# Kernel optimization log

Measured on AMD Instinct MI355X. Metric: run time of the kernel, lower is better.

Reference implementation:

```python
import jax, jax.numpy as jnp
import numpy as np

EPS = 1e-08
N_CODECS = 1024

def setup_inputs() -> dict:
    key = jax.random.key(0)
    indices = jax.random.randint(key, (16, 1048576), 0, N_CODECS, dtype=jnp.int64 if jax.config.jax_enable_x64 else jnp.int32)
    return {"indices": indices}

def reference(indices) -> jnp.ndarray:
    # Faithful to: encodings = eq(arange[:,None], flat[None,:]); probs = mean(encodings, dim=1)
    # mean of one-hot over N == count/N, so use a histogram (bincount) instead of the
    # O(n_codecs x N) boolean matrix.
    flat = indices.reshape(-1)
    counts = jnp.bincount(flat, length=N_CODECS)  # [n_codecs]
    probs = counts.astype(jnp.float32) / flat.shape[0]
    perplexity = jnp.exp(-jnp.sum(probs * jnp.log(probs + EPS)))
    return perplexity
```

## Files before the change

kernel.cpp:

```cpp
#include <hip/hip_runtime.h>
#include <hip/hip_bf16.h>

#define N_CODECS 1024
#define EPS 1e-8f

__global__ void zero_bins_kernel(unsigned int* __restrict__ gcounts) {
    int i = blockIdx.x * blockDim.x + threadIdx.x;
    if (i < N_CODECS) gcounts[i] = 0u;
}

__global__ void __launch_bounds__(256) hist_kernel(
        const int* __restrict__ idx,
        unsigned int* __restrict__ gcounts,
        int n4 ) {
    __shared__ unsigned int lcounts[N_CODECS];
    for (int i = threadIdx.x; i < N_CODECS; i += blockDim.x) lcounts[i] = 0u;
    __syncthreads();

    const int4* __restrict__ idx4 = (const int4*)idx;
    int stride = gridDim.x * blockDim.x;
    for (int i = blockIdx.x * blockDim.x + threadIdx.x; i < n4; i += stride) {
        int4 v = idx4[i];
        atomicAdd(&lcounts[v.x], 1u);
        atomicAdd(&lcounts[v.y], 1u);
        atomicAdd(&lcounts[v.z], 1u);
        atomicAdd(&lcounts[v.w], 1u);
    }
    __syncthreads();

    for (int i = threadIdx.x; i < N_CODECS; i += blockDim.x) {
        unsigned int c = lcounts[i];
        if (c) atomicAdd(&gcounts[i], c);
    }
}

__global__ void __launch_bounds__(1024) finalize_kernel(
        const unsigned int* __restrict__ gcounts,
        float* __restrict__ out,
        float invN) {
    int t = threadIdx.x;
    float p = (float)gcounts[t] * invN;
    float term = p * logf(p + EPS);

    #pragma unroll
    for (int off = 32; off > 0; off >>= 1) {
        term += __shfl_down(term, off, 64);
    }

    __shared__ float wsum[16];
    int wave = t >> 6;
    int lane = t & 63;
    if (lane == 0) wsum[wave] = term;
    __syncthreads();

    if (wave == 0) {
        float s = (lane < 16) ? wsum[lane] : 0.0f;
        #pragma unroll
        for (int off = 8; off > 0; off >>= 1) {
            s += __shfl_down(s, off, 64);
        }
        if (lane == 0) out[0] = expf(-s);
    }
}

extern "C" void kernel_launch(void* const* d_in, const int* in_sizes, int n_in,
                              void* d_out, int out_size, void* d_ws, size_t ws_size,
                              hipStream_t stream) {
    const int* indices = (const int*)d_in[0];
    int n = in_sizes[0];
    float* out = (float*)d_out;
    unsigned int* gcounts = (unsigned int*)d_ws;

    int n4 = n >> 2;

    zero_bins_kernel<<<(N_CODECS + 255) / 256, 256, 0, stream>>>(gcounts);

    hist_kernel<<<1024, 256, 0, stream>>>(indices, gcounts, n4);

    finalize_kernel<<<1, 1024, 0, stream>>>(gcounts, out, 1.0f / (float)n);
}
```

Measured before the change: 106.6 us.

## Replace global atomic merge with per-block partial histograms and tree reduction

Each histogram block now writes its full shared-memory histogram to its own slot in the workspace, with no global atomics. A new reduce kernel sums 64 partials per chunk into 16 chunk histograms, and finalize adds those 16. This drops the zero-bins launch and the contention from 1024 blocks atomically updating the same 1024 global counters. In exchange it writes 4 MB of partials, adds a reduction kernel launch, and needs a larger workspace.

```diff
diff --git a/kernel.cpp b/kernel.cpp
--- a/kernel.cpp
+++ b/kernel.cpp
@@ -3,23 +3,20 @@
 
 #define N_CODECS 1024
 #define EPS 1e-8f
+#define HIST_BLOCKS 1024
+#define CHUNKS 16
 
-__global__ void zero_bins_kernel(unsigned int* __restrict__ gcounts) {
-    int i = blockIdx.x * blockDim.x + threadIdx.x;
-    if (i < N_CODECS) gcounts[i] = 0u;
-}
-
-__global__ void __launch_bounds__(256) hist_kernel(
+__global__ void __launch_bounds__(256) hist_partial_kernel(
         const int* __restrict__ idx,
-        unsigned int* __restrict__ gcounts,
-        int n4 ) {
+        unsigned int* __restrict__ gpart,
+        int n4) {
     __shared__ unsigned int lcounts[N_CODECS];
-    for (int i = threadIdx.x; i < N_CODECS; i += blockDim.x) lcounts[i] = 0u;
+    for (int i = threadIdx.x; i < N_CODECS; i += 256) lcounts[i] = 0u;
     __syncthreads();
 
     const int4* __restrict__ idx4 = (const int4*)idx;
-    int stride = gridDim.x * blockDim.x;
-    for (int i = blockIdx.x * blockDim.x + threadIdx.x; i < n4; i += stride) {
+    int stride = gridDim.x * 256;
+    for (int i = blockIdx.x * 256 + threadIdx.x; i < n4; i += stride) {
         int4 v = idx4[i];
         atomicAdd(&lcounts[v.x], 1u);
         atomicAdd(&lcounts[v.y], 1u);
@@ -28,24 +25,47 @@
     }
     __syncthreads();
 
-    for (int i = threadIdx.x; i < N_CODECS; i += blockDim.x) {
-        unsigned int c = lcounts[i];
-        if (c) atomicAdd(&gcounts[i], c);
+    unsigned int* __restrict__ mypart = gpart + (size_t)blockIdx.x * N_CODECS;
+    #pragma unroll
+    for (int i = 0; i < N_CODECS / 256; ++i) {
+        int b = i * 256 + threadIdx.x;
+        mypart[b] = lcounts[b];
     }
 }
 
+__global__ void __launch_bounds__(256) reduce_kernel(
+        const unsigned int* __restrict__ gpart,
+        unsigned int* __restrict__ p2) {
+    int c = blockIdx.x >> 2;
+    int q = blockIdx.x & 3;
+    int bin = q * 256 + threadIdx.x;
+
+    const unsigned int* __restrict__ base = gpart + (size_t)(c * 64) * N_CODECS + bin;
+    unsigned int s0 = 0, s1 = 0, s2 = 0, s3 = 0;
+    #pragma unroll 4
+    for (int k = 0; k < 64; k += 4) {
+        s0 += base[(size_t)(k + 0) * N_CODECS];
+        s1 += base[(size_t)(k + 1) * N_CODECS];
+        s2 += base[(size_t)(k + 2) * N_CODECS];
+        s3 += base[(size_t)(k + 3) * N_CODECS];
+    }
+    p2[c * N_CODECS + bin] = s0 + s1 + s2 + s3;
+}
+
 __global__ void __launch_bounds__(1024) finalize_kernel(
-        const unsigned int* __restrict__ gcounts,
+        const unsigned int* __restrict__ p2,
         float* __restrict__ out,
         float invN) {
     int t = threadIdx.x;
-    float p = (float)gcounts[t] * invN;
+    unsigned int cnt = 0;
+    #pragma unroll
+    for (int c = 0; c < CHUNKS; ++c) cnt += p2[c * N_CODECS + t];
+
+    float p = (float)cnt * invN;
     float term = p * logf(p + EPS);
 
     #pragma unroll
-    for (int off = 32; off > 0; off >>= 1) {
-        term += __shfl_down(term, off, 64);
-    }
+    for (int off = 32; off > 0; off >>= 1) term += __shfl_down(term, off, 64);
 
     __shared__ float wsum[16];
     int wave = t >> 6;
@@ -56,9 +76,7 @@
     if (wave == 0) {
         float s = (lane < 16) ? wsum[lane] : 0.0f;
         #pragma unroll
-        for (int off = 8; off > 0; off >>= 1) {
-            s += __shfl_down(s, off, 64);
-        }
+        for (int off = 8; off > 0; off >>= 1) s += __shfl_down(s, off, 64);
         if (lane == 0) out[0] = expf(-s);
     }
 }
@@ -69,13 +87,13 @@
     const int* indices = (const int*)d_in[0];
     int n = in_sizes[0];
     float* out = (float*)d_out;
-    unsigned int* gcounts = (unsigned int*)d_ws;
+
+    unsigned int* gpart = (unsigned int*)d_ws;
+    unsigned int* p2    = gpart + (size_t)HIST_BLOCKS * N_CODECS;
 
     int n4 = n >> 2;
 
-    zero_bins_kernel<<<(N_CODECS + 255) / 256, 256, 0, stream>>>(gcounts);
-
-    hist_kernel<<<1024, 256, 0, stream>>>(indices, gcounts, n4);
-
-    finalize_kernel<<<1, 1024, 0, stream>>>(gcounts, out, 1.0f / (float)n);
+    hist_partial_kernel<<<HIST_BLOCKS, 256, 0, stream>>>(indices, gpart, n4);
+    reduce_kernel<<<CHUNKS * 4, 256, 0, stream>>>(gpart, p2);
+    finalize_kernel<<<1, 1024, 0, stream>>>(p2, out, 1.0f / (float)n);
 }
```

Measured after the change: 94.06 us. 1.13x faster.
